# Kernel tuning notes

Hardware: AMD Instinct MI355X
Metric: run time of the kernel (lower is better)

## Reference

```python
import jax, jax.numpy as jnp
import numpy as np

B, T, C, HD = 16, 2048, 1024, 64


def setup_inputs() -> dict:
    key = jax.random.key(0)
    kx, kk, kq, kv = jax.random.split(key, 4)
    x = jax.random.normal(kx, (B, T, C), dtype=jnp.float32)
    Wk = jax.random.normal(kk, (C, HD), dtype=jnp.float32) * (C ** -0.5)
    Wq = jax.random.normal(kq, (C, HD), dtype=jnp.float32) * (C ** -0.5)
    Wv = jax.random.normal(kv, (C, HD), dtype=jnp.float32) * (C ** -0.5)
    return {"x": x, "Wk": Wk, "Wq": Wq, "Wv": Wv}


def reference(x, Wk, Wq, Wv):
    Bs, Ts, Cs = x.shape
    k = x @ Wk  # [B,T,HD]
    q = x @ Wq
    v = x @ Wv
    # Faithful to original: scores = key @ query^T, scaled by 1/sqrt(C) (embed dim!)
    scores = jnp.einsum('bth,bsh->bts', k, q) / jnp.sqrt(jnp.float32(Cs))
    causal = jnp.tril(jnp.ones((Ts, Ts), dtype=bool))  # tril[:T,:T]
    scores = jnp.where(causal, scores, -jnp.inf)
    weights = jax.nn.softmax(scores, axis=-1)  # [B,T,T]
    return jnp.einsum('bts,bsh->bth', weights, v)  # [B,T,HD]
```

## Files before the change

kernel.cpp:

```cpp
#include <hip/hip_runtime.h>
#include <hip/hip_bf16.h>

#define B_ 16
#define T_ 2048
#define C_ 1024
#define HD_ 64

typedef __attribute__((ext_vector_type(8))) short bf16x8;
typedef __attribute__((ext_vector_type(4))) float f32x4;

__device__ __forceinline__ unsigned short f2bf(float f) {
  return __builtin_bit_cast(unsigned short, __float2bfloat16(f));
}

__device__ __forceinline__ bf16x8 cvt8(float4 a, float4 b) {
  bf16x8 r;
  r[0] = (short)f2bf(a.x); r[1] = (short)f2bf(a.y);
  r[2] = (short)f2bf(a.z); r[3] = (short)f2bf(a.w);
  r[4] = (short)f2bf(b.x); r[5] = (short)f2bf(b.y);
  r[6] = (short)f2bf(b.z); r[7] = (short)f2bf(b.w);
  return r;
}

__global__ void wconv_kernel(const float* __restrict__ Wk, const float* __restrict__ Wq,
                             const float* __restrict__ Wv, unsigned short* __restrict__ w3) {
  int o = blockIdx.x * 256 + threadIdx.x;
  if (o >= 16 * 12288) return;
  int kk = o / 12288;
  int n = o - kk * 12288;
  int row = n >> 6;
  int c = (n >> 3) & 7;
  int e = n & 7;
  int k = kk * 64 + (((c ^ (row & 7)) << 3) | e);
  int m = row >> 6, d = row & 63;
  const float* W = (m == 0) ? Wk : (m == 1) ? Wq : Wv;
  float v = W[k * HD_ + d];
  if (m == 0) v *= 0.03125f * 1.44269504088896f;
  w3[o] = f2bf(v);
}

__global__ __launch_bounds__(512, 2) void qkv_kernel(const float* __restrict__ x,
                                                     const unsigned short* __restrict__ w3,
                                                     unsigned short* __restrict__ kb,
                                                     unsigned short* __restrict__ qb,
                                                     unsigned short* __restrict__ vb) {
  __shared__ __align__(16) unsigned short wl[2 * 12288];

  const int tid = threadIdx.x;
  const int lane = tid & 63;
  const int w = tid >> 6;
  const int l15 = lane & 15, lh = lane >> 4;
  const int r0 = blockIdx.x * 128;

  const float* xp = x + (size_t)(r0 + w * 16 + l15) * C_ + lh * 8;
  const int fb0 = l15 * 64 + ((lh ^ (l15 & 7)) << 3);
  const int fb1 = l15 * 64 + (((4 | lh) ^ (l15 & 7)) << 3);

  f32x4 acc[12];
#pragma unroll
  for (int i = 0; i < 12; ++i) acc[i] = {0.f, 0.f, 0.f, 0.f};

  float4 xa0, xa1, xa2, xa3, xb0, xb1, xb2, xb3;

#define STAGE(BUF, KK)                                                              \
  do {                                                                              \
    _Pragma("unroll")                                                               \
    for (int i_ = 0; i_ < 3; ++i_) {                                                \
      const int eo_ = ((w * 3 + i_) << 9) + lane * 8;    \
      __builtin_amdgcn_global_load_lds(                                             \
          (const __attribute__((address_space(1))) void*)(w3 + (KK) * 12288 + eo_), \
          (__attribute__((address_space(3))) void*)&wl[(BUF) * 12288 + eo_],        \
          16, 0, 0);                                                                \
    }                                                                               \
  } while (0)

#define XLOADA(KK) do { const float* p_ = xp + (KK) * 64;                      \
    xa0 = *(const float4*)(p_);      xa1 = *(const float4*)(p_ + 4);           \
    xa2 = *(const float4*)(p_ + 32); xa3 = *(const float4*)(p_ + 36); } while (0)
#define XLOADB(KK) do { const float* p_ = xp + (KK) * 64;                      \
    xb0 = *(const float4*)(p_);      xb1 = *(const float4*)(p_ + 4);           \
    xb2 = *(const float4*)(p_ + 32); xb3 = *(const float4*)(p_ + 36); } while (0)

#define COMPUTE(BUF, X0, X1, X2, X3)                                                \
  do {                                                                              \
    bf16x8 a0 = cvt8(X0, X1);                                                       \
    bf16x8 a1 = cvt8(X2, X3);                                                       \
    _Pragma("unroll")                                                               \
    for (int f_ = 0; f_ < 12; ++f_) {                                               \
      bf16x8 b0 = *(const bf16x8*)&wl[(BUF) * 12288 + f_ * 1024 + fb0];             \
      acc[f_] = __builtin_amdgcn_mfma_f32_16x16x32_bf16(a0, b0, acc[f_], 0, 0, 0);  \
      bf16x8 b1 = *(const bf16x8*)&wl[(BUF) * 12288 + f_ * 1024 + fb1];             \
      acc[f_] = __builtin_amdgcn_mfma_f32_16x16x32_bf16(a1, b1, acc[f_], 0, 0, 0);  \
    }                                                                               \
  } while (0)

#define SB __builtin_amdgcn_sched_barrier(0)
#define WAIT(VM)                                                  \
  do {                                                            \
    SB;                                                           \
    asm volatile("s_waitcnt vmcnt(" #VM ")" ::: "memory");        \
    SB;                                                           \
    __builtin_amdgcn_s_barrier();                                 \
  } while (0)

  STAGE(0, 0);
  SB;
  XLOADA(0);
  SB;

#pragma unroll 1
  for (int it = 0; it < 7; ++it) {
    const int k2 = it * 2;
    STAGE(1, k2 + 1);
    SB;
    XLOADB(k2 + 1);
    WAIT(7);
    COMPUTE(0, xa0, xa1, xa2, xa3);
    __builtin_amdgcn_s_barrier();
    STAGE(0, k2 + 2);
    SB;
    XLOADA(k2 + 2);
    WAIT(7);
    COMPUTE(1, xb0, xb1, xb2, xb3);
    __builtin_amdgcn_s_barrier();
  }
  STAGE(1, 15);
  SB;
  XLOADB(15);
  WAIT(7);
  COMPUTE(0, xa0, xa1, xa2, xa3);
  __builtin_amdgcn_s_barrier();
  WAIT(0);
  COMPUTE(1, xb0, xb1, xb2, xb3);

#undef WAIT
#undef SB
#undef COMPUTE
#undef XLOADB
#undef XLOADA
#undef STAGE

#pragma unroll
  for (int cf = 0; cf < 4; ++cf) {
    int col = cf * 16 + l15;
#pragma unroll
    for (int r = 0; r < 4; ++r) {
      size_t row = (size_t)(r0 + w * 16 + lh * 4 + r);
      kb[row * HD_ + col] = f2bf(acc[cf][r]);
      qb[row * HD_ + col] = f2bf(acc[4 + cf][r]);
      vb[row * HD_ + col] = f2bf(acc[8 + cf][r]);
    }
  }
}

__global__ __launch_bounds__(256) void attn_kernel(const unsigned short* __restrict__ kb,
                                                   const unsigned short* __restrict__ qb,
                                                   const unsigned short* __restrict__ vb,
                                                   float* __restrict__ out) {
  __shared__ __align__(16) unsigned short q_lds[2][64 * 72];
  __shared__ __align__(16) unsigned short v_lds[2][64 * 72];
  __shared__ __align__(16) unsigned short p_lds[64 * 72];

  const int tid = threadIdx.x;
  const int lane = tid & 63;
  const int w = tid >> 6;
  const int bid = blockIdx.x;
  const int idx = bid >> 4;
  const int jt = (idx < 16) ? (31 - idx) : (idx - 16);
  const int b = bid & 15;
  const int t0 = jt * 64;
  const int l15 = lane & 15;
  const int lh = lane >> 4;
  const size_t base = (size_t)b * T_ * HD_;

  const int qrow = tid >> 3, qc8 = tid & 7;
  const int vss = tid & 63, vd0 = (tid >> 6) * 8;

  bf16x8 kf[2];
#pragma unroll
  for (int ks = 0; ks < 2; ++ks)
    kf[ks] = *reinterpret_cast<const bf16x8*>(
        &kb[base + (size_t)(t0 + w * 16 + l15) * HD_ + ks * 32 + lh * 8]);

  bf16x8 qr0, qr1, vr0, vr1;
  qr0 = *reinterpret_cast<const bf16x8*>(&qb[base + (size_t)qrow * HD_ + qc8 * 8]);
  qr1 = *reinterpret_cast<const bf16x8*>(&qb[base + (size_t)(qrow + 32) * HD_ + qc8 * 8]);
  vr0 = *reinterpret_cast<const bf16x8*>(&vb[base + (size_t)vss * HD_ + vd0]);
  vr1 = *reinterpret_cast<const bf16x8*>(&vb[base + (size_t)vss * HD_ + vd0 + 32]);

  f32x4 o[4];
#pragma unroll
  for (int i = 0; i < 4; ++i) o[i] = {0.f, 0.f, 0.f, 0.f};
  float mrun[4], lrun[4];
#pragma unroll
  for (int r = 0; r < 4; ++r) { mrun[r] = -1e30f; lrun[r] = 0.f; }

  for (int j = 0; j <= jt; ++j) {
    const int buf = j & 1;
    *reinterpret_cast<bf16x8*>(&q_lds[buf][qrow * 72 + qc8 * 8]) = qr0;
    *reinterpret_cast<bf16x8*>(&q_lds[buf][(qrow + 32) * 72 + qc8 * 8]) = qr1;
#pragma unroll
    for (int jj = 0; jj < 8; ++jj) v_lds[buf][(vd0 + jj) * 72 + vss] = (unsigned short)vr0[jj];
#pragma unroll
    for (int jj = 0; jj < 8; ++jj) v_lds[buf][(vd0 + 32 + jj) * 72 + vss] = (unsigned short)vr1[jj];
    __syncthreads();

    if (j < jt) {
      const size_t sb = base + (size_t)(j + 1) * 64 * HD_;
      qr0 = *reinterpret_cast<const bf16x8*>(&qb[sb + (size_t)qrow * HD_ + qc8 * 8]);
      qr1 = *reinterpret_cast<const bf16x8*>(&qb[sb + (size_t)(qrow + 32) * HD_ + qc8 * 8]);
      vr0 = *reinterpret_cast<const bf16x8*>(&vb[sb + (size_t)vss * HD_ + vd0]);
      vr1 = *reinterpret_cast<const bf16x8*>(&vb[sb + (size_t)vss * HD_ + vd0 + 32]);
    }
    __builtin_amdgcn_sched_barrier(0);

    f32x4 sf[4];
#pragma unroll
    for (int cf = 0; cf < 4; ++cf) sf[cf] = {0.f, 0.f, 0.f, 0.f};
    __builtin_amdgcn_s_setprio(1);
#pragma unroll
    for (int ks = 0; ks < 2; ++ks) {
#pragma unroll
      for (int cf = 0; cf < 4; ++cf) {
        bf16x8 bq = *reinterpret_cast<const bf16x8*>(&q_lds[buf][(cf * 16 + l15) * 72 + ks * 32 + lh * 8]);
        sf[cf] = __builtin_amdgcn_mfma_f32_16x16x32_bf16(kf[ks], bq, sf[cf], 0, 0, 0);
      }
    }
    __builtin_amdgcn_s_setprio(0);

    const bool diag = (j == jt);
    const int s0 = j * 64;
    float pv[4][4];
#pragma unroll
    for (int r = 0; r < 4; ++r) {
      const int tg = t0 + w * 16 + lh * 4 + r;
      float pm = -1e30f;
#pragma unroll
      for (int cf = 0; cf < 4; ++cf) {
        float v = sf[cf][r];
        if (diag && (s0 + cf * 16 + l15) > tg) v = -1e30f;
        pv[cf][r] = v;
        pm = fmaxf(pm, v);
      }
      pm = fmaxf(pm, __shfl_xor(pm, 1));
      pm = fmaxf(pm, __shfl_xor(pm, 2));
      pm = fmaxf(pm, __shfl_xor(pm, 4));
      pm = fmaxf(pm, __shfl_xor(pm, 8));
      float mn = fmaxf(mrun[r], pm);
      float scl = exp2f(mrun[r] - mn);
      mrun[r] = mn;
      float rs = 0.f;
#pragma unroll
      for (int cf = 0; cf < 4; ++cf) {
        float e = exp2f(pv[cf][r] - mn);
        pv[cf][r] = e;
        rs += e;
      }
      rs += __shfl_xor(rs, 1);
      rs += __shfl_xor(rs, 2);
      rs += __shfl_xor(rs, 4);
      rs += __shfl_xor(rs, 8);
      lrun[r] = lrun[r] * scl + rs;
#pragma unroll
      for (int df = 0; df < 4; ++df) o[df][r] *= scl;
    }
#pragma unroll
    for (int cf = 0; cf < 4; ++cf)
#pragma unroll
      for (int r = 0; r < 4; ++r)
        p_lds[(w * 16 + lh * 4 + r) * 72 + cf * 16 + l15] = f2bf(pv[cf][r]);

    __builtin_amdgcn_s_setprio(1);
#pragma unroll
    for (int ks = 0; ks < 2; ++ks) {
      bf16x8 pa = *reinterpret_cast<const bf16x8*>(&p_lds[(w * 16 + l15) * 72 + ks * 32 + lh * 8]);
#pragma unroll
      for (int df = 0; df < 4; ++df) {
        bf16x8 bv = *reinterpret_cast<const bf16x8*>(&v_lds[buf][(df * 16 + l15) * 72 + ks * 32 + lh * 8]);
        o[df] = __builtin_amdgcn_mfma_f32_16x16x32_bf16(pa, bv, o[df], 0, 0, 0);
      }
    }
    __builtin_amdgcn_s_setprio(0);
  }

#pragma unroll
  for (int r = 0; r < 4; ++r) {
    float inv = 1.f / lrun[r];
    int row = t0 + w * 16 + lh * 4 + r;
#pragma unroll
    for (int df = 0; df < 4; ++df)
      out[base + (size_t)row * HD_ + df * 16 + l15] = o[df][r] * inv;
  }
}

extern "C" void kernel_launch(void* const* d_in, const int* in_sizes, int n_in,
                              void* d_out, int out_size, void* d_ws, size_t ws_size,
                              hipStream_t stream) {
  const float* x  = (const float*)d_in[0];
  const float* Wk = (const float*)d_in[1];
  const float* Wq = (const float*)d_in[2];
  const float* Wv = (const float*)d_in[3];
  float* out = (float*)d_out;

  char* ws = (char*)d_ws;
  unsigned short* w3 = (unsigned short*)ws;
  unsigned short* kb = (unsigned short*)(ws + 524288);
  unsigned short* qb = (unsigned short*)(ws + 524288 + 4 * 1024 * 1024);
  unsigned short* vb = (unsigned short*)(ws + 524288 + 8 * 1024 * 1024);

  hipLaunchKernelGGL(wconv_kernel, dim3(768), dim3(256), 0, stream, Wk, Wq, Wv, w3);
  hipLaunchKernelGGL(qkv_kernel, dim3(256), dim3(512), 0, stream, x, w3, kb, qb, vb);
  hipLaunchKernelGGL(attn_kernel, dim3(512), dim3(256), 0, stream, kb, qb, vb, out);
}
```

Before: 97.96 us.

## Restructure QKV projection to stage x through LDS with 128-wide K panels

The QKV projection now processes K in 8 panels of 128 instead of 16 of 64, with the weight layout regenerated to match. Each x tile is loaded with row-coalesced float4 reads, converted to bf16 and written into a swizzled LDS buffer, and MFMA A-fragments are then read from LDS instead of per-lane strided global loads. The aim is better global coalescing for x and fewer barrier/sync rounds. In exchange it uses 128KB of LDS and a launch bound of 1 block per CU, which cuts occupancy and adds LDS write traffic plus a full vmcnt(0) wait each panel.

```diff
diff --git a/kernel.cpp b/kernel.cpp
--- a/kernel.cpp
+++ b/kernel.cpp
@@ -13,132 +13,130 @@
   return __builtin_bit_cast(unsigned short, __float2bfloat16(f));
 }
 
-__device__ __forceinline__ bf16x8 cvt8(float4 a, float4 b) {
-  bf16x8 r;
-  r[0] = (short)f2bf(a.x); r[1] = (short)f2bf(a.y);
-  r[2] = (short)f2bf(a.z); r[3] = (short)f2bf(a.w);
-  r[4] = (short)f2bf(b.x); r[5] = (short)f2bf(b.y);
-  r[6] = (short)f2bf(b.z); r[7] = (short)f2bf(b.w);
-  return r;
-}
-
 __global__ void wconv_kernel(const float* __restrict__ Wk, const float* __restrict__ Wq,
-                             const float* __restrict__ Wv, unsigned short* __restrict__ w3) {
+                             const float* __restrict__ Wv, unsigned short* __restrict__ w8) {
   int o = blockIdx.x * 256 + threadIdx.x;
-  if (o >= 16 * 12288) return;
-  int kk = o / 12288;
-  int n = o - kk * 12288;
-  int row = n >> 6;
-  int c = (n >> 3) & 7;
+  if (o >= 196608) return;
+  int p = o / 24576;
+  int n = o - p * 24576;
+  int row = n >> 7;
+  int pc = (n >> 3) & 15;
   int e = n & 7;
-  int k = kk * 64 + (((c ^ (row & 7)) << 3) | e);
+  int c = pc ^ (row & 7);
+  int k = p * 128 + c * 8 + e;
   int m = row >> 6, d = row & 63;
   const float* W = (m == 0) ? Wk : (m == 1) ? Wq : Wv;
   float v = W[k * HD_ + d];
   if (m == 0) v *= 0.03125f * 1.44269504088896f;
-  w3[o] = f2bf(v);
-}
-
-__global__ __launch_bounds__(512, 2) void qkv_kernel(const float* __restrict__ x,
-                                                     const unsigned short* __restrict__ w3,
+  w8[o] = f2bf(v);
+}
+
+__global__ __launch_bounds__(512, 1) void qkv_kernel(const float* __restrict__ x,
+                                                     const unsigned short* __restrict__ w8,
                                                      unsigned short* __restrict__ kb,
                                                      unsigned short* __restrict__ qb,
                                                      unsigned short* __restrict__ vb) {
-  __shared__ __align__(16) unsigned short wl[2 * 12288];
+  __shared__ __align__(16) unsigned short lds[65536];
 
   const int tid = threadIdx.x;
   const int lane = tid & 63;
   const int w = tid >> 6;
   const int l15 = lane & 15, lh = lane >> 4;
   const int r0 = blockIdx.x * 128;
-
-  const float* xp = x + (size_t)(r0 + w * 16 + l15) * C_ + lh * 8;
-  const int fb0 = l15 * 64 + ((lh ^ (l15 & 7)) << 3);
-  const int fb1 = l15 * 64 + (((4 | lh) ^ (l15 & 7)) << 3);
+  const int xbase = 49152 + w * 2048;
+  const int ro = lane >> 5, q = lane & 31;
 
   f32x4 acc[12];
 #pragma unroll
   for (int i = 0; i < 12; ++i) acc[i] = {0.f, 0.f, 0.f, 0.f};
 
-  float4 xa0, xa1, xa2, xa3, xb0, xb1, xb2, xb3;
-
-#define STAGE(BUF, KK)                                                              \
-  do {                                                                              \
-    _Pragma("unroll")                                                               \
-    for (int i_ = 0; i_ < 3; ++i_) {                                                \
-      const int eo_ = ((w * 3 + i_) << 9) + lane * 8;    \
-      __builtin_amdgcn_global_load_lds(                                             \
-          (const __attribute__((address_space(1))) void*)(w3 + (KK) * 12288 + eo_), \
-          (__attribute__((address_space(3))) void*)&wl[(BUF) * 12288 + eo_],        \
-          16, 0, 0);                                                                \
-    }                                                                               \
+  float4 xr[8];
+
+#define STAGEW(BUF, P)                                                                \
+  do {                                                                                \
+    _Pragma("unroll")                                                                 \
+    for (int i_ = 0; i_ < 6; ++i_) {                                                  \
+      const int eo_ = i_ * 4096 + tid * 8;                                            \
+      __builtin_amdgcn_global_load_lds(                                               \
+          (const __attribute__((address_space(1))) void*)(w8 + (P) * 24576 + eo_),    \
+          (__attribute__((address_space(3))) void*)&lds[(BUF) * 24576 + eo_],         \
+          16, 0, 0);                                                                  \
+    }                                                                                 \
   } while (0)
 
-#define XLOADA(KK) do { const float* p_ = xp + (KK) * 64;                      \
-    xa0 = *(const float4*)(p_);      xa1 = *(const float4*)(p_ + 4);           \
-    xa2 = *(const float4*)(p_ + 32); xa3 = *(const float4*)(p_ + 36); } while (0)
-#define XLOADB(KK) do { const float* p_ = xp + (KK) * 64;                      \
-    xb0 = *(const float4*)(p_);      xb1 = *(const float4*)(p_ + 4);           \
-    xb2 = *(const float4*)(p_ + 32); xb3 = *(const float4*)(p_ + 36); } while (0)
-
-#define COMPUTE(BUF, X0, X1, X2, X3)                                                \
-  do {                                                                              \
-    bf16x8 a0 = cvt8(X0, X1);                                                       \
-    bf16x8 a1 = cvt8(X2, X3);                                                       \
-    _Pragma("unroll")                                                               \
-    for (int f_ = 0; f_ < 12; ++f_) {                                               \
-      bf16x8 b0 = *(const bf16x8*)&wl[(BUF) * 12288 + f_ * 1024 + fb0];             \
-      acc[f_] = __builtin_amdgcn_mfma_f32_16x16x32_bf16(a0, b0, acc[f_], 0, 0, 0);  \
-      bf16x8 b1 = *(const bf16x8*)&wl[(BUF) * 12288 + f_ * 1024 + fb1];             \
-      acc[f_] = __builtin_amdgcn_mfma_f32_16x16x32_bf16(a1, b1, acc[f_], 0, 0, 0);  \
-    }                                                                               \
+#define XLOAD(P)                                                                      \
+  do {                                                                                \
+    const float* bp_ = x + (size_t)(r0 + w * 16 + ro) * C_ + (P) * 128 + q * 4;       \
+    _Pragma("unroll")                                                                 \
+    for (int j_ = 0; j_ < 8; ++j_)                                                    \
+      xr[j_] = *(const float4*)(bp_ + (size_t)(j_ * 2) * C_);                         \
   } while (0)
 
+#define XWRITE()                                                                      \
+  do {                                                                                \
+    _Pragma("unroll")                                                                 \
+    for (int j_ = 0; j_ < 8; ++j_) {                                                  \
+      const int row_ = j_ * 2 + ro;                                                   \
+      const int idx_ = xbase + row_ * 128 + (((q >> 1) ^ (row_ & 7)) << 3) + (q & 1) * 4; \
+      ushort4 hv_;                                                                    \
+      hv_.x = f2bf(xr[j_].x); hv_.y = f2bf(xr[j_].y);                                 \
+      hv_.z = f2bf(xr[j_].z); hv_.w = f2bf(xr[j_].w);                                 \
+      *(ushort4*)&lds[idx_] = hv_;                                                    \
+    }                                                                                 \
+  } while (0)
+
+#define COMPUTE(WB)                                                                   \
+  do {                                                                                \
+    _Pragma("unroll")                                                                 \
+    for (int kk_ = 0; kk_ < 4; ++kk_) {                                               \
+      const int sc_ = ((kk_ * 4 + lh) ^ (l15 & 7)) << 3;                              \
+      bf16x8 a_ = *(const bf16x8*)&lds[xbase + l15 * 128 + sc_];                      \
+      _Pragma("unroll")                                                               \
+      for (int cf_ = 0; cf_ < 12; ++cf_) {                                            \
+        bf16x8 b_ = *(const bf16x8*)&lds[(WB) + (cf_ * 16 + l15) * 128 + sc_];        \
+        acc[cf_] = __builtin_amdgcn_mfma_f32_16x16x32_bf16(a_, b_, acc[cf_], 0, 0, 0);\
+      }                                                                               \
+    }                                                                                 \
+  } while (0)
+
 #define SB __builtin_amdgcn_sched_barrier(0)
-#define WAIT(VM)                                                  \
-  do {                                                            \
-    SB;                                                           \
-    asm volatile("s_waitcnt vmcnt(" #VM ")" ::: "memory");        \
-    SB;                                                           \
-    __builtin_amdgcn_s_barrier();                                 \
-  } while (0)
-
-  STAGE(0, 0);
+
+  STAGEW(0, 0);
   SB;
-  XLOADA(0);
+  XLOAD(0);
   SB;
+  asm volatile("s_waitcnt vmcnt(0)" ::: "memory");
+  SB;
+  XWRITE();
+  __builtin_amdgcn_s_barrier();
 
 #pragma unroll 1
-  for (int it = 0; it < 7; ++it) {
-    const int k2 = it * 2;
-    STAGE(1, k2 + 1);
-    SB;
-    XLOADB(k2 + 1);
-    WAIT(7);
-    COMPUTE(0, xa0, xa1, xa2, xa3);
-    __builtin_amdgcn_s_barrier();
-    STAGE(0, k2 + 2);
-    SB;
-    XLOADA(k2 + 2);
-    WAIT(7);
-    COMPUTE(1, xb0, xb1, xb2, xb3);
-    __builtin_amdgcn_s_barrier();
+  for (int p = 0; p < 8; ++p) {
+    const int wb = (p & 1) * 24576;
+    if (p < 7) {
+      XLOAD(p + 1);
+      SB;
+      STAGEW((p + 1) & 1, p + 1);
+      SB;
+    }
+    COMPUTE(wb);
+    if (p < 7) {
+      SB;
+      asm volatile("s_waitcnt vmcnt(6)" ::: "memory");
+      SB;
+      XWRITE();
+      SB;
+      asm volatile("s_waitcnt vmcnt(0)" ::: "memory");
+      SB;
+      __builtin_amdgcn_s_barrier();
+    }
   }
-  STAGE(1, 15);
-  SB;
-  XLOADB(15);
-  WAIT(7);
-  COMPUTE(0, xa0, xa1, xa2, xa3);
-  __builtin_amdgcn_s_barrier();
-  WAIT(0);
-  COMPUTE(1, xb0, xb1, xb2, xb3);
-
-#undef WAIT
+
 #undef SB
 #undef COMPUTE
-#undef XLOADB
-#undef XLOADA
-#undef STAGE
+#undef XWRITE
+#undef XLOAD
+#undef STAGEW
 
 #pragma unroll
   for (int cf = 0; cf < 4; ++cf) {
@@ -303,12 +301,12 @@
   float* out = (float*)d_out;
 
   char* ws = (char*)d_ws;
-  unsigned short* w3 = (unsigned short*)ws;
+  unsigned short* w8 = (unsigned short*)ws;
   unsigned short* kb = (unsigned short*)(ws + 524288);
   unsigned short* qb = (unsigned short*)(ws + 524288 + 4 * 1024 * 1024);
   unsigned short* vb = (unsigned short*)(ws + 524288 + 8 * 1024 * 1024);
 
-  hipLaunchKernelGGL(wconv_kernel, dim3(768), dim3(256), 0, stream, Wk, Wq, Wv, w3);
-  hipLaunchKernelGGL(qkv_kernel, dim3(256), dim3(512), 0, stream, x, w3, kb, qb, vb);
+  hipLaunchKernelGGL(wconv_kernel, dim3(768), dim3(256), 0, stream, Wk, Wq, Wv, w8);
+  hipLaunchKernelGGL(qkv_kernel, dim3(256), dim3(512), 0, stream, x, w8, kb, qb, vb);
   hipLaunchKernelGGL(attn_kernel, dim3(512), dim3(256), 0, stream, kb, qb, vb, out);
 }
```

After: 92.20 us. 1.06x faster.

## Stage x through LDS as bf16 with coalesced row loads and smaller blocks

Applied to the files above, without the earlier changes.

The QKV projection kernel now loads x rows with fully coalesced per-row float4 loads, converts them to bf16 and writes them into a swizzled LDS buffer in quarter-K chunks. MFMA A-operands are then read from LDS instead of being converted from registers on every k-step. Blocks shrink to 64 rows and 256 threads, the grid doubles to 512, and each wave stages twice as many weight chunks. The aim is better global access coalescing for x and more blocks to hide latency. The cost is the periodic x prologue, which runs unoverlapped with compute, plus extra LDS traffic and syncs per k-step.

```diff
diff --git a/kernel.cpp b/kernel.cpp
--- a/kernel.cpp
+++ b/kernel.cpp
@@ -11,15 +11,6 @@
 
 __device__ __forceinline__ unsigned short f2bf(float f) {
   return __builtin_bit_cast(unsigned short, __float2bfloat16(f));
-}
-
-__device__ __forceinline__ bf16x8 cvt8(float4 a, float4 b) {
-  bf16x8 r;
-  r[0] = (short)f2bf(a.x); r[1] = (short)f2bf(a.y);
-  r[2] = (short)f2bf(a.z); r[3] = (short)f2bf(a.w);
-  r[4] = (short)f2bf(b.x); r[5] = (short)f2bf(b.y);
-  r[6] = (short)f2bf(b.z); r[7] = (short)f2bf(b.w);
-  return r;
 }
 
 __global__ void wconv_kernel(const float* __restrict__ Wk, const float* __restrict__ Wq,
@@ -39,20 +30,22 @@
   w3[o] = f2bf(v);
 }
 
-__global__ __launch_bounds__(512, 2) void qkv_kernel(const float* __restrict__ x,
+__global__ __launch_bounds__(256, 2) void qkv_kernel(const float* __restrict__ x,
                                                      const unsigned short* __restrict__ w3,
                                                      unsigned short* __restrict__ kb,
                                                      unsigned short* __restrict__ qb,
                                                      unsigned short* __restrict__ vb) {
+  __shared__ __align__(16) unsigned short xls[16384];
   __shared__ __align__(16) unsigned short wl[2 * 12288];
 
   const int tid = threadIdx.x;
   const int lane = tid & 63;
   const int w = tid >> 6;
   const int l15 = lane & 15, lh = lane >> 4;
-  const int r0 = blockIdx.x * 128;
-
-  const float* xp = x + (size_t)(r0 + w * 16 + l15) * C_ + lh * 8;
+  const int r0 = blockIdx.x * 64;
+  const int xw = w * 4096;
+  const int abase = xw + l15 * 256;
+  const int aswz = (l15 & 7) << 3;
   const int fb0 = l15 * 64 + ((lh ^ (l15 & 7)) << 3);
   const int fb1 = l15 * 64 + (((4 | lh) ^ (l15 & 7)) << 3);
 
@@ -60,85 +53,91 @@
 #pragma unroll
   for (int i = 0; i < 12; ++i) acc[i] = {0.f, 0.f, 0.f, 0.f};
 
-  float4 xa0, xa1, xa2, xa3, xb0, xb1, xb2, xb3;
-
-#define STAGE(BUF, KK)                                                              \
-  do {                                                                              \
-    _Pragma("unroll")                                                               \
-    for (int i_ = 0; i_ < 3; ++i_) {                                                \
-      const int eo_ = ((w * 3 + i_) << 9) + lane * 8;    \
-      __builtin_amdgcn_global_load_lds(                                             \
-          (const __attribute__((address_space(1))) void*)(w3 + (KK) * 12288 + eo_), \
-          (__attribute__((address_space(3))) void*)&wl[(BUF) * 12288 + eo_],        \
-          16, 0, 0);                                                                \
-    }                                                                               \
-  } while (0)
-
-#define XLOADA(KK) do { const float* p_ = xp + (KK) * 64;                      \
-    xa0 = *(const float4*)(p_);      xa1 = *(const float4*)(p_ + 4);           \
-    xa2 = *(const float4*)(p_ + 32); xa3 = *(const float4*)(p_ + 36); } while (0)
-#define XLOADB(KK) do { const float* p_ = xp + (KK) * 64;                      \
-    xb0 = *(const float4*)(p_);      xb1 = *(const float4*)(p_ + 4);           \
-    xb2 = *(const float4*)(p_ + 32); xb3 = *(const float4*)(p_ + 36); } while (0)
-
-#define COMPUTE(BUF, X0, X1, X2, X3)                                                \
-  do {                                                                              \
-    bf16x8 a0 = cvt8(X0, X1);                                                       \
-    bf16x8 a1 = cvt8(X2, X3);                                                       \
-    _Pragma("unroll")                                                               \
-    for (int f_ = 0; f_ < 12; ++f_) {                                               \
-      bf16x8 b0 = *(const bf16x8*)&wl[(BUF) * 12288 + f_ * 1024 + fb0];             \
-      acc[f_] = __builtin_amdgcn_mfma_f32_16x16x32_bf16(a0, b0, acc[f_], 0, 0, 0);  \
-      bf16x8 b1 = *(const bf16x8*)&wl[(BUF) * 12288 + f_ * 1024 + fb1];             \
-      acc[f_] = __builtin_amdgcn_mfma_f32_16x16x32_bf16(a1, b1, acc[f_], 0, 0, 0);  \
-    }                                                                               \
-  } while (0)
+  float4 xq[8];
 
 #define SB __builtin_amdgcn_sched_barrier(0)
-#define WAIT(VM)                                                  \
-  do {                                                            \
-    SB;                                                           \
-    asm volatile("s_waitcnt vmcnt(" #VM ")" ::: "memory");        \
-    SB;                                                           \
-    __builtin_amdgcn_s_barrier();                                 \
-  } while (0)
-
-  STAGE(0, 0);
-  SB;
-  XLOADA(0);
-  SB;
-
-#pragma unroll 1
-  for (int it = 0; it < 7; ++it) {
-    const int k2 = it * 2;
-    STAGE(1, k2 + 1);
-    SB;
-    XLOADB(k2 + 1);
-    WAIT(7);
-    COMPUTE(0, xa0, xa1, xa2, xa3);
-    __builtin_amdgcn_s_barrier();
-    STAGE(0, k2 + 2);
-    SB;
-    XLOADA(k2 + 2);
-    WAIT(7);
-    COMPUTE(1, xb0, xb1, xb2, xb3);
-    __builtin_amdgcn_s_barrier();
-  }
-  STAGE(1, 15);
-  SB;
-  XLOADB(15);
-  WAIT(7);
-  COMPUTE(0, xa0, xa1, xa2, xa3);
-  __builtin_amdgcn_s_barrier();
-  WAIT(0);
-  COMPUTE(1, xb0, xb1, xb2, xb3);
-
-#undef WAIT
+
+#define XISSUE(R) xq[(R) & 7] = *(const float4*)(xb + (size_t)(R) * C_ + lane * 4)
+
+#define XPROC(R, VM)                                                                   \
+  do {                                                                                 \
+    SB;                                                                                \
+    asm volatile("s_waitcnt vmcnt(" #VM ")" ::: "memory");                             \
+    SB;                                                                                \
+    ushort4 h4_;                                                                       \
+    h4_.x = f2bf(xq[(R) & 7].x); h4_.y = f2bf(xq[(R) & 7].y);                          \
+    h4_.z = f2bf(xq[(R) & 7].z); h4_.w = f2bf(xq[(R) & 7].w);                          \
+    *(ushort4*)&xls[xw + (R) * 256 + ((lane * 4) ^ (((R) & 7) << 3))] = h4_;           \
+  } while (0)
+
+#define XPRO(H)                                                                        \
+  do {                                                                                 \
+    const float* xb = x + (size_t)(r0 + w * 16) * C_ + (H) * 256;                      \
+    XISSUE(0); XISSUE(1); XISSUE(2); XISSUE(3);                                        \
+    XISSUE(4); XISSUE(5); XISSUE(6); XISSUE(7);                                        \
+    XPROC(0, 7); XISSUE(8);  XPROC(1, 7); XISSUE(9);                                   \
+    XPROC(2, 7); XISSUE(10); XPROC(3, 7); XISSUE(11);                                  \
+    XPROC(4, 7); XISSUE(12); XPROC(5, 7); XISSUE(13);                                  \
+    XPROC(6, 7); XISSUE(14); XPROC(7, 7); XISSUE(15);                                  \
+    XPROC(8, 7); XPROC(9, 6); XPROC(10, 5); XPROC(11, 4);                              \
+    XPROC(12, 3); XPROC(13, 2); XPROC(14, 1); XPROC(15, 0);                            \
+  } while (0)
+
+#define STAGEW(KK, BUF)                                                                \
+  do {                                                                                 \
+    _Pragma("unroll")                                                                  \
+    for (int i_ = 0; i_ < 6; ++i_) {                                                   \
+      const int eo_ = ((w * 6 + i_) << 9) + lane * 8;                                  \
+      __builtin_amdgcn_global_load_lds(                                                \
+          (const __attribute__((address_space(1))) void*)(w3 + (KK) * 12288 + eo_),    \
+          (__attribute__((address_space(3))) void*)&wl[(BUF) * 12288 + eo_],           \
+          16, 0, 0);                                                                   \
+    }                                                                                  \
+  } while (0)
+
+#define COMPUTE(CUR, KKL)                                                              \
+  do {                                                                                 \
+    _Pragma("unroll")                                                                  \
+    for (int ks_ = 0; ks_ < 2; ++ks_) {                                                \
+      const int kl_ = (KKL) * 64 + ks_ * 32 + lh * 8;                                  \
+      bf16x8 a_ = *(const bf16x8*)&xls[abase + (kl_ ^ aswz)];                          \
+      const int fb_ = ks_ ? fb1 : fb0;                                                 \
+      _Pragma("unroll")                                                                \
+      for (int cf_ = 0; cf_ < 12; ++cf_) {                                             \
+        bf16x8 b_ = *(const bf16x8*)&wl[(CUR) * 12288 + cf_ * 1024 + fb_];             \
+        acc[cf_] = __builtin_amdgcn_mfma_f32_16x16x32_bf16(a_, b_, acc[cf_], 0, 0, 0); \
+      }                                                                                \
+    }                                                                                  \
+  } while (0)
+
+#define KSTEP(KKG, VM)                                                                 \
+  do {                                                                                 \
+    __syncthreads();                             \
+    if ((KKG) < 15) STAGEW((KKG) + 1, ((KKG) + 1) & 1);                                \
+    SB;                                                                                \
+    asm volatile("s_waitcnt vmcnt(" #VM ")" ::: "memory");                             \
+    SB;                                                                                \
+    __builtin_amdgcn_s_barrier();                    \
+    COMPUTE((KKG) & 1, (KKG) & 3);                                                     \
+  } while (0)
+
+  XPRO(0);
+  STAGEW(0, 0);
+  KSTEP(0, 6);  KSTEP(1, 6);  KSTEP(2, 6);  KSTEP(3, 6);
+  XPRO(1);
+  KSTEP(4, 6);  KSTEP(5, 6);  KSTEP(6, 6);  KSTEP(7, 6);
+  XPRO(2);
+  KSTEP(8, 6);  KSTEP(9, 6);  KSTEP(10, 6); KSTEP(11, 6);
+  XPRO(3);
+  KSTEP(12, 6); KSTEP(13, 6); KSTEP(14, 6); KSTEP(15, 0);
+
+#undef KSTEP
+#undef COMPUTE
+#undef STAGEW
+#undef XPRO
+#undef XPROC
+#undef XISSUE
 #undef SB
-#undef COMPUTE
-#undef XLOADB
-#undef XLOADA
-#undef STAGE
 
 #pragma unroll
   for (int cf = 0; cf < 4; ++cf) {
@@ -309,6 +308,6 @@
   unsigned short* vb = (unsigned short*)(ws + 524288 + 8 * 1024 * 1024);
 
   hipLaunchKernelGGL(wconv_kernel, dim3(768), dim3(256), 0, stream, Wk, Wq, Wv, w3);
-  hipLaunchKernelGGL(qkv_kernel, dim3(256), dim3(512), 0, stream, x, w3, kb, qb, vb);
+  hipLaunchKernelGGL(qkv_kernel, dim3(512), dim3(256), 0, stream, x, w3, kb, qb, vb);
   hipLaunchKernelGGL(attn_kernel, dim3(512), dim3(256), 0, stream, kb, qb, vb, out);
 }
```

After: 97.43 us. No clear change (-0.5%).
